# Kernel tuning notes

Hardware: AMD Instinct MI355X
Metric: run time of the kernel (lower is better)

## Reference

```python
import jax, jax.numpy as jnp
import numpy as np

N_EXPERTS = 8
D_MODEL = 512
HIDDEN = 1408
TOTAL_TOKENS = 32768  # 4096 tokens per expert, equal contiguous segments


def setup_inputs() -> dict:
    key = jax.random.key(0)
    k1, k2, k3 = jax.random.split(key, 3)
    sorted_x = jax.random.normal(k1, (TOTAL_TOKENS, D_MODEL), dtype=jnp.float32)
    # weights init: normal(std=0.02) as in the torch module
    w12 = 0.02 * jax.random.normal(k2, (N_EXPERTS, 2 * HIDDEN, D_MODEL), dtype=jnp.float32)
    w3 = 0.02 * jax.random.normal(k3, (N_EXPERTS, D_MODEL, HIDDEN), dtype=jnp.float32)
    tpe = TOTAL_TOKENS // N_EXPERTS
    expert_starts = jnp.arange(N_EXPERTS, dtype=jnp.int32) * tpe
    expert_ends = expert_starts + tpe
    return {"sorted_x": sorted_x, "w12": w12, "w3": w3,
            "expert_starts": expert_starts, "expert_ends": expert_ends}


def reference(sorted_x, w12, w3, expert_starts, expert_ends):
    """Grouped SwiGLU expert MLP over tokens pre-sorted by expert.

    setup_inputs() produces equal-sized contiguous expert segments, so each
    expert processes tpe = T // E tokens (fixed-size grouped GEMM).
    """
    E, twoH, D = w12.shape
    T = sorted_x.shape[0]
    tpe = T // E  # tokens per expert segment

    # gather each expert's contiguous token block: (E, tpe, D)
    x_e = jax.vmap(lambda s: jax.lax.dynamic_slice(sorted_x, (s, 0), (tpe, D)))(expert_starts)

    # grouped GEMM 1 (fused gate+up): (E, tpe, 2H)
    h12 = jnp.einsum('etd,ehd->eth', x_e, w12).astype(jnp.float32)
    h1, h2 = jnp.split(h12, 2, axis=-1)
    h = jax.nn.silu(h1) * h2  # SwiGLU

    # grouped GEMM 2 (down-proj): (E, tpe, D)
    out = jnp.einsum('eth,edh->etd', h.astype(sorted_x.dtype), w3).astype(jnp.float32)
    # segments are contiguous and in expert order -> concat == reshape
    return out.reshape(T, D)
```

## Files before the change

### kernel.cpp

```cpp
#include <hip/hip_runtime.h>
#include <stdint.h>

#define TPE 4096
#define DM 512
#define HID 1408
#define NE 8

typedef unsigned short u16;
typedef __attribute__((ext_vector_type(8))) __bf16 bf16x8;
typedef __attribute__((ext_vector_type(4))) float f32x4;

__device__ __forceinline__ u16 f2bf(float f) {
  union { float f; uint32_t u; } v; v.f = f;
  uint32_t u = v.u;
  u += 0x7fffu + ((u >> 16) & 1u);
  return (u16)(u >> 16);
}

__global__ void cvt_f32_bf16(const float* __restrict__ in, u16* __restrict__ out, int n4) {
  int i = blockIdx.x * blockDim.x + threadIdx.x;
  if (i >= n4) return;
  float4 v = reinterpret_cast<const float4*>(in)[i];
  union { u16 s[4]; uint2 u2; } o;
  o.s[0] = f2bf(v.x); o.s[1] = f2bf(v.y); o.s[2] = f2bf(v.z); o.s[3] = f2bf(v.w);
  reinterpret_cast<uint2*>(out)[i] = o.u2;
}

__device__ __forceinline__ void stage_tile(u16* lds, const u16* g, int lda,
                                           int wave, int lane) {
#pragma unroll
  for (int r = 0; r < 2; ++r) {
    const u16* gp = g + (size_t)((r * 64 + wave * 16) + (lane >> 2)) * lda + (lane & 3) * 8;
    u16* lp = lds + (r * 64 + wave * 16) * 32;
    __builtin_amdgcn_global_load_lds((const __attribute__((address_space(1))) void*)gp,
                                     (__attribute__((address_space(3))) void*)lp,
                                     16, 0, 0);
  }
}

__global__ __launch_bounds__(256, 2)
void gemm1_swiglu(const u16* __restrict__ xb, const u16* __restrict__ w12b,
                  u16* __restrict__ hb) {
  __shared__ u16 sA[128 * 32];
  __shared__ u16 sBg[128 * 32];
  __shared__ u16 sBu[128 * 32];
  const int mt = blockIdx.x, nt = blockIdx.y, e = blockIdx.z;
  const int tid = threadIdx.x, wave = tid >> 6, lane = tid & 63;
  const int wm = wave >> 1, wn = wave & 1;
  const int quad = lane >> 4, rr = lane & 15;

  const u16* A  = xb + (size_t)(e * TPE + mt * 128) * DM;
  const u16* Bg = w12b + (size_t)e * (2 * HID) * DM + (size_t)(nt * 128) * DM;
  const u16* Bu = Bg + (size_t)HID * DM;

  f32x4 zero = {0.f, 0.f, 0.f, 0.f};
  f32x4 accg[4][4], accu[4][4];
#pragma unroll
  for (int i = 0; i < 4; ++i)
#pragma unroll
    for (int j = 0; j < 4; ++j) { accg[i][j] = zero; accu[i][j] = zero; }

  for (int k0 = 0; k0 < DM; k0 += 32) {
    stage_tile(sA, A + k0, DM, wave, lane);
    stage_tile(sBg, Bg + k0, DM, wave, lane);
    stage_tile(sBu, Bu + k0, DM, wave, lane);
    __syncthreads();

    bf16x8 af[4], bg[4], bu[4];
#pragma unroll
    for (int mi = 0; mi < 4; ++mi)
      af[mi] = *reinterpret_cast<const bf16x8*>(&sA[(wm * 64 + mi * 16 + rr) * 32 + quad * 8]);
#pragma unroll
    for (int ni = 0; ni < 4; ++ni) {
      bg[ni] = *reinterpret_cast<const bf16x8*>(&sBg[(wn * 64 + ni * 16 + rr) * 32 + quad * 8]);
      bu[ni] = *reinterpret_cast<const bf16x8*>(&sBu[(wn * 64 + ni * 16 + rr) * 32 + quad * 8]);
    }
#pragma unroll
    for (int mi = 0; mi < 4; ++mi)
#pragma unroll
      for (int ni = 0; ni < 4; ++ni) {
        accg[mi][ni] = __builtin_amdgcn_mfma_f32_16x16x32_bf16(af[mi], bg[ni], accg[mi][ni], 0, 0, 0);
        accu[mi][ni] = __builtin_amdgcn_mfma_f32_16x16x32_bf16(af[mi], bu[ni], accu[mi][ni], 0, 0, 0);
      }
    __syncthreads();
  }

  const size_t rowbase = (size_t)(e * TPE + mt * 128 + wm * 64);
  const int colbase = nt * 128 + wn * 64;
#pragma unroll
  for (int mi = 0; mi < 4; ++mi)
#pragma unroll
    for (int ni = 0; ni < 4; ++ni)
#pragma unroll
      for (int r2 = 0; r2 < 4; ++r2) {
        float g = accg[mi][ni][r2];
        float u = accu[mi][ni][r2];
        float s = (g / (1.f + __expf(-g))) * u;
        size_t row = rowbase + mi * 16 + quad * 4 + r2;
        int col = colbase + ni * 16 + rr;
        hb[row * HID + col] = f2bf(s);
      }
}

__global__ __launch_bounds__(256, 2)
void gemm2(const u16* __restrict__ hb, const u16* __restrict__ w3b,
           float* __restrict__ out) {
  __shared__ u16 sA[128 * 32];
  __shared__ u16 sB[128 * 32];
  const int mt = blockIdx.x, nt = blockIdx.y, e = blockIdx.z;
  const int tid = threadIdx.x, wave = tid >> 6, lane = tid & 63;
  const int wm = wave >> 1, wn = wave & 1;
  const int quad = lane >> 4, rr = lane & 15;

  const u16* A = hb + (size_t)(e * TPE + mt * 128) * HID;
  const u16* B = w3b + (size_t)e * DM * HID + (size_t)(nt * 128) * HID;

  f32x4 zero = {0.f, 0.f, 0.f, 0.f};
  f32x4 acc[4][4];
#pragma unroll
  for (int i = 0; i < 4; ++i)
#pragma unroll
    for (int j = 0; j < 4; ++j) acc[i][j] = zero;

  for (int k0 = 0; k0 < HID; k0 += 32) {
    stage_tile(sA, A + k0, HID, wave, lane);
    stage_tile(sB, B + k0, HID, wave, lane);
    __syncthreads();

    bf16x8 af[4], bf[4];
#pragma unroll
    for (int mi = 0; mi < 4; ++mi)
      af[mi] = *reinterpret_cast<const bf16x8*>(&sA[(wm * 64 + mi * 16 + rr) * 32 + quad * 8]);
#pragma unroll
    for (int ni = 0; ni < 4; ++ni)
      bf[ni] = *reinterpret_cast<const bf16x8*>(&sB[(wn * 64 + ni * 16 + rr) * 32 + quad * 8]);
#pragma unroll
    for (int mi = 0; mi < 4; ++mi)
#pragma unroll
      for (int ni = 0; ni < 4; ++ni)
        acc[mi][ni] = __builtin_amdgcn_mfma_f32_16x16x32_bf16(af[mi], bf[ni], acc[mi][ni], 0, 0, 0);
    __syncthreads();
  }

  const size_t rowbase = (size_t)(e * TPE + mt * 128 + wm * 64);
  const int colbase = nt * 128 + wn * 64;
#pragma unroll
  for (int mi = 0; mi < 4; ++mi)
#pragma unroll
    for (int ni = 0; ni < 4; ++ni)
#pragma unroll
      for (int r2 = 0; r2 < 4; ++r2) {
        size_t row = rowbase + mi * 16 + quad * 4 + r2;
        int col = colbase + ni * 16 + rr;
        out[row * DM + col] = acc[mi][ni][r2];
      }
}

extern "C" void kernel_launch(void* const* d_in, const int* in_sizes, int n_in,
                              void* d_out, int out_size, void* d_ws, size_t ws_size,
                              hipStream_t stream) {
  (void)in_sizes; (void)n_in; (void)out_size; (void)ws_size;
  const float* x   = (const float*)d_in[0];
  const float* w12 = (const float*)d_in[1];
  const float* w3  = (const float*)d_in[2];
  float* out = (float*)d_out;

  char* ws = (char*)d_ws;
  u16* xb   = (u16*)(ws);
  u16* w12b = (u16*)(ws + (size_t)33554432);
  u16* w3b  = (u16*)(ws + (size_t)33554432 + 23068672);
  u16* hb   = (u16*)(ws + (size_t)33554432 + 23068672 + 11534336);

  const int n4x   = (32768 * 512) / 4;
  const int n4w12 = (NE * 2816 * 512) / 4;
  const int n4w3  = (NE * 512 * 1408) / 4;
  cvt_f32_bf16<<<n4x / 256, 256, 0, stream>>>(x, xb, n4x);
  cvt_f32_bf16<<<n4w12 / 256, 256, 0, stream>>>(w12, w12b, n4w12);
  cvt_f32_bf16<<<n4w3 / 256, 256, 0, stream>>>(w3, w3b, n4w3);

  gemm1_swiglu<<<dim3(32, 11, NE), 256, 0, stream>>>(xb, w12b, hb);
  gemm2<<<dim3(32, 4, NE), 256, 0, stream>>>(hb, w3b, out);
}
```

Baseline: 349.2 us.

## Double K-tile depth to 64 and XOR-swizzle LDS layout to avoid bank conflicts

```diff
diff --git a/kernel.cpp b/kernel.cpp
--- a/kernel.cpp
+++ b/kernel.cpp
@@ -26,24 +26,31 @@
   reinterpret_cast<uint2*>(out)[i] = o.u2;
 }
 
-__device__ __forceinline__ void stage_tile(u16* lds, const u16* g, int lda,
-                                           int wave, int lane) {
+__device__ __forceinline__ void stage_tile64(u16* lds, const u16* g, int lda,
+                                             int wave, int lane) {
+  const int srow = lane >> 3;
+  const int gchunk = (lane & 7) ^ srow;
 #pragma unroll
-  for (int r = 0; r < 2; ++r) {
-    const u16* gp = g + (size_t)((r * 64 + wave * 16) + (lane >> 2)) * lda + (lane & 3) * 8;
-    u16* lp = lds + (r * 64 + wave * 16) * 32;
+  for (int r = 0; r < 4; ++r) {
+    const int row0 = (wave * 4 + r) * 8;
+    const u16* gp = g + (size_t)(row0 + srow) * lda + gchunk * 8;
+    u16* lp = lds + row0 * 64;
     __builtin_amdgcn_global_load_lds((const __attribute__((address_space(1))) void*)gp,
                                      (__attribute__((address_space(3))) void*)lp,
                                      16, 0, 0);
   }
 }
 
+__device__ __forceinline__ bf16x8 read_frag(const u16* lds, int row, int kchunk) {
+  return *reinterpret_cast<const bf16x8*>(&lds[row * 64 + (((kchunk ^ (row & 7)) << 3))]);
+}
+
 __global__ __launch_bounds__(256, 2)
 void gemm1_swiglu(const u16* __restrict__ xb, const u16* __restrict__ w12b,
                   u16* __restrict__ hb) {
-  __shared__ u16 sA[128 * 32];
-  __shared__ u16 sBg[128 * 32];
-  __shared__ u16 sBu[128 * 32];
+  __shared__ u16 sA[128 * 64];
+  __shared__ u16 sBg[128 * 64];
+  __shared__ u16 sBu[128 * 64];
   const int mt = blockIdx.x, nt = blockIdx.y, e = blockIdx.z;
   const int tid = threadIdx.x, wave = tid >> 6, lane = tid & 63;
   const int wm = wave >> 1, wn = wave & 1;
@@ -60,28 +67,32 @@
 #pragma unroll
     for (int j = 0; j < 4; ++j) { accg[i][j] = zero; accu[i][j] = zero; }
 
-  for (int k0 = 0; k0 < DM; k0 += 32) {
-    stage_tile(sA, A + k0, DM, wave, lane);
-    stage_tile(sBg, Bg + k0, DM, wave, lane);
-    stage_tile(sBu, Bu + k0, DM, wave, lane);
+  for (int k0 = 0; k0 < DM; k0 += 64) {
+    stage_tile64(sA, A + k0, DM, wave, lane);
+    stage_tile64(sBg, Bg + k0, DM, wave, lane);
+    stage_tile64(sBu, Bu + k0, DM, wave, lane);
     __syncthreads();
 
-    bf16x8 af[4], bg[4], bu[4];
 #pragma unroll
-    for (int mi = 0; mi < 4; ++mi)
-      af[mi] = *reinterpret_cast<const bf16x8*>(&sA[(wm * 64 + mi * 16 + rr) * 32 + quad * 8]);
+    for (int kk = 0; kk < 2; ++kk) {
+      const int kc = kk * 4 + quad;
+      bf16x8 af[4], bg[4], bu[4];
 #pragma unroll
-    for (int ni = 0; ni < 4; ++ni) {
-      bg[ni] = *reinterpret_cast<const bf16x8*>(&sBg[(wn * 64 + ni * 16 + rr) * 32 + quad * 8]);
-      bu[ni] = *reinterpret_cast<const bf16x8*>(&sBu[(wn * 64 + ni * 16 + rr) * 32 + quad * 8]);
-    }
-#pragma unroll
-    for (int mi = 0; mi < 4; ++mi)
+      for (int mi = 0; mi < 4; ++mi)
+        af[mi] = read_frag(sA, wm * 64 + mi * 16 + rr, kc);
 #pragma unroll
       for (int ni = 0; ni < 4; ++ni) {
-        accg[mi][ni] = __builtin_amdgcn_mfma_f32_16x16x32_bf16(af[mi], bg[ni], accg[mi][ni], 0, 0, 0);
-        accu[mi][ni] = __builtin_amdgcn_mfma_f32_16x16x32_bf16(af[mi], bu[ni], accu[mi][ni], 0, 0, 0);
+        bg[ni] = read_frag(sBg, wn * 64 + ni * 16 + rr, kc);
+        bu[ni] = read_frag(sBu, wn * 64 + ni * 16 + rr, kc);
       }
+#pragma unroll
+      for (int mi = 0; mi < 4; ++mi)
+#pragma unroll
+        for (int ni = 0; ni < 4; ++ni) {
+          accg[mi][ni] = __builtin_amdgcn_mfma_f32_16x16x32_bf16(af[mi], bg[ni], accg[mi][ni], 0, 0, 0);
+          accu[mi][ni] = __builtin_amdgcn_mfma_f32_16x16x32_bf16(af[mi], bu[ni], accu[mi][ni], 0, 0, 0);
+        }
+    }
     __syncthreads();
   }
 
@@ -105,8 +116,8 @@
 __global__ __launch_bounds__(256, 2)
 void gemm2(const u16* __restrict__ hb, const u16* __restrict__ w3b,
            float* __restrict__ out) {
-  __shared__ u16 sA[128 * 32];
-  __shared__ u16 sB[128 * 32];
+  __shared__ u16 sA[128 * 64];
+  __shared__ u16 sB[128 * 64];
   const int mt = blockIdx.x, nt = blockIdx.y, e = blockIdx.z;
   const int tid = threadIdx.x, wave = tid >> 6, lane = tid & 63;
   const int wm = wave >> 1, wn = wave & 1;
@@ -122,23 +133,27 @@
 #pragma unroll
     for (int j = 0; j < 4; ++j) acc[i][j] = zero;
 
-  for (int k0 = 0; k0 < HID; k0 += 32) {
-    stage_tile(sA, A + k0, HID, wave, lane);
-    stage_tile(sB, B + k0, HID, wave, lane);
+  for (int k0 = 0; k0 < HID; k0 += 64) {
+    stage_tile64(sA, A + k0, HID, wave, lane);
+    stage_tile64(sB, B + k0, HID, wave, lane);
     __syncthreads();
 
-    bf16x8 af[4], bf[4];
 #pragma unroll
-    for (int mi = 0; mi < 4; ++mi)
-      af[mi] = *reinterpret_cast<const bf16x8*>(&sA[(wm * 64 + mi * 16 + rr) * 32 + quad * 8]);
+    for (int kk = 0; kk < 2; ++kk) {
+      const int kc = kk * 4 + quad;
+      bf16x8 af[4], bfr[4];
 #pragma unroll
-    for (int ni = 0; ni < 4; ++ni)
-      bf[ni] = *reinterpret_cast<const bf16x8*>(&sB[(wn * 64 + ni * 16 + rr) * 32 + quad * 8]);
-#pragma unroll
-    for (int mi = 0; mi < 4; ++mi)
+      for (int mi = 0; mi < 4; ++mi)
+        af[mi] = read_frag(sA, wm * 64 + mi * 16 + rr, kc);
 #pragma unroll
       for (int ni = 0; ni < 4; ++ni)
-        acc[mi][ni] = __builtin_amdgcn_mfma_f32_16x16x32_bf16(af[mi], bf[ni], acc[mi][ni], 0, 0, 0);
+        bfr[ni] = read_frag(sB, wn * 64 + ni * 16 + rr, kc);
+#pragma unroll
+      for (int mi = 0; mi < 4; ++mi)
+#pragma unroll
+        for (int ni = 0; ni < 4; ++ni)
+          acc[mi][ni] = __builtin_amdgcn_mfma_f32_16x16x32_bf16(af[mi], bfr[ni], acc[mi][ni], 0, 0, 0);
+    }
     __syncthreads();
   }
 
```

After: 336.4 us. 3.6% less time.
